# Kernel tuning notes

Measured on AMD Instinct MI355X. Metric: run time of the kernel, lower is better.

Reference implementation:

```python
import jax, jax.numpy as jnp
import numpy as np

B, S, N, E = 2048, 5, 80, 592
FX, FF, FE, D = 8, 4, 8, 8
H = 800  # GRU hidden


def setup_inputs() -> dict:
    key = jax.random.key(0)
    ks = jax.random.split(key, 20)
    inp = {
        "x": jax.random.normal(ks[0], (B, S, N, FX), jnp.float32),
        "edge_index": jax.random.randint(ks[1], (B, S, 2, E), 0, N, jnp.int32),
        "edge_f": jax.random.normal(ks[2], (B, S, E, FF), jnp.float32),
        "edge_attr": jax.random.normal(ks[3], (B, S, E, FE), jnp.float32),
        # GNN (net_ResEG) params
        "Wx": jax.random.normal(ks[4], (FX, D), jnp.float32) * 0.1,
        "We": jax.random.normal(ks[5], (FE, D), jnp.float32) * 0.1,
        "Wf": jax.random.normal(ks[6], (FF, D), jnp.float32) * 0.1,
        "Wedge": jax.random.normal(ks[7], (2 * D + FE, D), jnp.float32) * 0.1,
        # GRU params (PyTorch layout: [3H, in])
        "w_ih": jax.random.normal(ks[8], (3 * H, N * D + E * D), jnp.float32) * 0.02,
        "w_hh": jax.random.normal(ks[9], (3 * H, H), jnp.float32) * 0.02,
        "b_ih": jnp.zeros((3 * H,), jnp.float32),
        "b_hh": jnp.zeros((3 * H,), jnp.float32),
        # MLP params
        "mlp_w1": jax.random.normal(ks[10], (S * H, 1280), jnp.float32) * 0.02,
        "mlp_b1": jnp.zeros((1280,), jnp.float32),
        "mlp_w2": jax.random.normal(ks[11], (1280, S * 80), jnp.float32) * 0.02,
        "mlp_b2": jnp.zeros((S * 80,), jnp.float32),
    }
    return inp


def _gnn(xg, eig, efg, eag, Wx, We, Wf, Wedge):
    # one graph: xg [N,FX], eig [2,E], efg [E,FF], eag [E,FE]
    src, dst = eig[0], eig[1]
    m = jax.nn.relu(eag @ We + efg @ Wf)            # [E,D] edge messages
    agg = jnp.zeros((N, D), m.dtype).at[dst].add(m)  # scatter-add to nodes
    x_out = xg + jax.nn.relu(xg @ Wx + agg)          # residual node update [N,D]
    feat = jnp.concatenate([x_out[src], x_out[dst], eag], axis=-1)  # [E,2D+FE]
    e_out = eag + jax.nn.relu(feat @ Wedge)          # residual edge update [E,D]
    return x_out, e_out


def _forward(x, edge_index, edge_f, edge_attr, Wx, We, Wf, Wedge,
             w_ih, w_hh, b_ih, b_hh, mlp_w1, mlp_b1, mlp_w2, mlp_b2):
    # normalize edge indices (edge_index[i,j] - edge_index[i,j,0].min())
    mins = edge_index[:, :, 0, :].min(axis=-1)[:, :, None, None]  # [B,S,1,1]
    ei = edge_index - mins

    flat = lambda a: a.reshape((B * S,) + a.shape[2:])
    x1, e1 = jax.vmap(lambda a, b, c, d: _gnn(a, b, c, d, Wx, We, Wf, Wedge))(
        flat(x), flat(ei), flat(edge_f), flat(edge_attr))
    x1 = x1.reshape(B, S, N * D)
    e1 = e1.reshape(B, S, E * D)
    seq = jnp.concatenate([x1, e1], axis=2)  # [B,S,5376]

    # single-layer GRU, batch_first (dropout inactive for 1 layer)
    def step(h, xt):
        gi = xt @ w_ih.T + b_ih   # [B,3H]
        gh = h @ w_hh.T + b_hh
        ir, iz, inn = jnp.split(gi, 3, axis=-1)
        hr, hz, hn = jnp.split(gh, 3, axis=-1)
        r = jax.nn.sigmoid(ir + hr)
        z = jax.nn.sigmoid(iz + hz)
        n = jnp.tanh(inn + r * hn)
        h_new = (1.0 - z) * n + z * h
        return h_new, h_new

    h0 = jnp.zeros((B, H), seq.dtype)
    _, ys = jax.lax.scan(step, h0, jnp.swapaxes(seq, 0, 1))  # [S,B,H]
    y = jnp.swapaxes(ys, 0, 1).reshape(B, S * H)             # [B,4000]

    y = y @ mlp_w1 + mlp_b1
    y = y @ mlp_w2 + mlp_b2
    return y.reshape(B, 80, 5)


def reference(x, edge_index, edge_f, edge_attr, Wx, We, Wf, Wedge,
              w_ih, w_hh, b_ih, b_hh, mlp_w1, mlp_b1, mlp_w2, mlp_b2):
    return _forward(x, edge_index, edge_f, edge_attr, Wx, We, Wf, Wedge,
                    w_ih, w_hh, b_ih, b_hh, mlp_w1, mlp_b1, mlp_w2, mlp_b2)
```

## Files before the change

kernel.cpp:

```cpp
#include <hip/hip_runtime.h>
#include <math.h>

constexpr int B_  = 2048;
constexpr int S_  = 5;
constexpr int N_  = 80;
constexpr int E_  = 592;
constexpr int FX_ = 8;
constexpr int FF_ = 4;
constexpr int FE_ = 8;
constexpr int D_  = 8;
constexpr int H_  = 800;

constexpr int BS_  = B_ * S_;
constexpr int XD_  = N_ * D_;
constexpr int ED_  = E_ * D_;
constexpr int SEQ_ = XD_ + ED_;
constexpr int G3_  = 3 * H_;
constexpr int MIN_ = S_ * H_;
constexpr int MH_  = 1280;
constexpr int MO_  = S_ * 80;

typedef __bf16 bf16_t;
typedef __bf16 bf16x8 __attribute__((ext_vector_type(8)));
typedef float  f32x4  __attribute__((ext_vector_type(4)));

__device__ __forceinline__ float sigmoidf_(float x) {
    return 1.0f / (1.0f + expf(-x));
}

__device__ __forceinline__ void async16(const void* g, void* l) {
    __builtin_amdgcn_global_load_lds(
        (const __attribute__((address_space(1))) unsigned int*)g,
        (__attribute__((address_space(3))) unsigned int*)l,
        16, 0, 0);
}

__global__ __launch_bounds__(256, 4) void gnn_kernel(
    const float* __restrict__ x,
    const int*   __restrict__ ei,
    const float* __restrict__ ef,
    const float* __restrict__ ea,
    const float* __restrict__ Wx,
    const float* __restrict__ We,
    const float* __restrict__ Wf,
    const float* __restrict__ Wedge,
    bf16_t* __restrict__ seq)
{
    const int tid  = threadIdx.x;
    const int w    = tid >> 6;
    const int lane = tid & 63;
    const int g    = blockIdx.x * 4 + w;

    __shared__ float sWx[FX_ * D_];
    __shared__ float sWe[FE_ * D_];
    __shared__ float sWf[FF_ * D_];
    __shared__ float sWedge[24 * D_];
    __shared__ float agg[4][D_ * N_];
    __shared__ float su [4][D_ * N_];
    __shared__ float sv [4][D_ * N_];

    if (tid < 64) { sWx[tid] = Wx[tid]; sWe[tid] = We[tid]; }
    if (tid < 32) sWf[tid] = Wf[tid];
    if (tid < 192) sWedge[tid] = Wedge[tid];

    float* aggw = agg[w];
    float* uw   = su[w];
    float* vw   = sv[w];
    for (int i = lane; i < D_ * N_; i += 64) aggw[i] = 0.0f;

    const int* srcp = ei + (size_t)g * 2 * E_;
    const int* dstp = srcp + E_;

    int lmin = 0x7fffffff;
    for (int e = lane; e < E_; e += 64) lmin = min(lmin, srcp[e]);
    #pragma unroll
    for (int off = 32; off; off >>= 1)
        lmin = min(lmin, __shfl_xor(lmin, off, 64));
    const int mn = lmin;

    __syncthreads();

    const float* eag = ea + (size_t)g * E_ * FE_;
    const float* efg = ef + (size_t)g * E_ * FF_;
    for (int e = lane; e < E_; e += 64) {
        const float4* ap = (const float4*)(eag + (size_t)e * FE_);
        float4 a0 = ap[0], a1 = ap[1];
        float4 f0 = *(const float4*)(efg + (size_t)e * FF_);
        float a[FE_] = {a0.x, a0.y, a0.z, a0.w, a1.x, a1.y, a1.z, a1.w};
        float fv[FF_] = {f0.x, f0.y, f0.z, f0.w};

        int dadj = dstp[e] - mn;
        if (dadj < 0) dadj += N_;

        #pragma unroll
        for (int d = 0; d < D_; d++) {
            float m = 0.0f;
            #pragma unroll
            for (int k = 0; k < FE_; k++) m += a[k] * sWe[k * D_ + d];
            #pragma unroll
            for (int k = 0; k < FF_; k++) m += fv[k] * sWf[k * D_ + d];
            atomicAdd(&aggw[d * N_ + dadj], fmaxf(m, 0.0f));
        }
    }
    __syncthreads();

    const float* xg = x + (size_t)g * N_ * FX_;
    bf16_t* seqrow = seq + (size_t)g * SEQ_;
    for (int n = lane; n < N_; n += 64) {
        const float4* xp = (const float4*)(xg + (size_t)n * FX_);
        float4 x0 = xp[0], x1 = xp[1];
        float xi[FX_] = {x0.x, x0.y, x0.z, x0.w, x1.x, x1.y, x1.z, x1.w};

        float xo[D_];
        bf16x8 pk;
        #pragma unroll
        for (int d = 0; d < D_; d++) {
            float v = aggw[d * N_ + n];
            #pragma unroll
            for (int k = 0; k < FX_; k++) v += xi[k] * sWx[k * D_ + d];
            xo[d] = xi[d] + fmaxf(v, 0.0f);
            pk[d] = (bf16_t)xo[d];
        }
        *(bf16x8*)(seqrow + (size_t)n * D_) = pk;

        #pragma unroll
        for (int d = 0; d < D_; d++) {
            float uu = 0.0f, vv = 0.0f;
            #pragma unroll
            for (int k = 0; k < D_; k++) {
                uu += xo[k] * sWedge[k * D_ + d];
                vv += xo[k] * sWedge[(D_ + k) * D_ + d];
            }
            uw[d * N_ + n] = uu;
            vw[d * N_ + n] = vv;
        }
    }
    __syncthreads();

    for (int e = lane; e < E_; e += 64) {
        const float4* ap = (const float4*)(eag + (size_t)e * FE_);
        float4 a0 = ap[0], a1 = ap[1];
        float a[FE_] = {a0.x, a0.y, a0.z, a0.w, a1.x, a1.y, a1.z, a1.w};

        int sadj = srcp[e] - mn;
        int dadj = dstp[e] - mn;
        if (dadj < 0) dadj += N_;

        bf16x8 pk;
        #pragma unroll
        for (int d = 0; d < D_; d++) {
            float t = uw[d * N_ + sadj] + vw[d * N_ + dadj];
            #pragma unroll
            for (int k = 0; k < FE_; k++) t += a[k] * sWedge[(2 * D_ + k) * D_ + d];
            pk[d] = (bf16_t)(a[d] + fmaxf(t, 0.0f));
        }
        *(bf16x8*)(seqrow + XD_ + (size_t)e * D_) = pk;
    }
}

template <int TBK, typename OutT>
__global__ __launch_bounds__(256) void gemm2ph(
    const bf16_t* __restrict__ A,
    const bf16_t* __restrict__ Bm,
    const float*  __restrict__ bias,
    OutT* __restrict__ C,
    int M, int Nn, int K)
{
    constexpr int GR  = TBK / 8;
    constexpr int GM  = GR - 1;
    constexpr int RPI = 256 / GR;
    constexpr int NISS = 128 / RPI;
    constexpr int KK  = TBK / 32;

    __shared__ bf16_t As[2][128 * TBK];
    __shared__ bf16_t Bs[2][128 * TBK];

    const int tid  = threadIdx.x;
    const int wave = tid >> 6;
    const int lane = tid & 63;

    const int nbx = gridDim.x;
    int swz = blockIdx.x;
    if ((nbx & 7) == 0) {
        int cpx = nbx >> 3;
        swz = (swz & 7) * cpx + (swz >> 3);
    }
    const int ntn = (Nn + 127) >> 7;
    const int m0 = (swz / ntn) * 128;
    const int n0 = (swz % ntn) * 128;

    const int wm = (wave & 1) * 64;
    const int wn = (wave >> 1) * 64;

    const int r_loc  = tid / GR;
    const int s_slot = tid % GR;

    const int fr = lane & 15;
    const int fq = lane >> 4;

    f32x4 acc[4][4] = {};
    const int nkt = K / TBK;

    auto STAGE = [&](int t, int buf) {
        const size_t k0 = (size_t)t * TBK;
        #pragma unroll
        for (int i = 0; i < NISS; i++) {
            int row = i * RPI + r_loc;
            int gsl = s_slot ^ (row & GM);
            async16(A + (size_t)(m0 + row) * K + k0 + gsl * 8,
                    &As[buf][row * TBK + s_slot * 8]);
        }
        #pragma unroll
        for (int i = 0; i < NISS; i++) {
            int row = i * RPI + r_loc;
            int gsl = s_slot ^ (row & GM);
            int br = n0 + row; if (br > Nn - 1) br = Nn - 1;
            async16(Bm + (size_t)br * K + k0 + gsl * 8,
                    &Bs[buf][row * TBK + s_slot * 8]);
        }
    };

    STAGE(0, 0);
    asm volatile("s_waitcnt vmcnt(0)" ::: "memory");
    __builtin_amdgcn_sched_barrier(0);
    __builtin_amdgcn_s_barrier();

    for (int t = 0; t < nkt; ++t) {
        const int c = t & 1;
        int tn = t + 1; if (tn > nkt - 1) tn = nkt - 1;
        STAGE(tn, c ^ 1);

        const bf16_t* Ab = As[c];
        const bf16_t* Bb = Bs[c];
        bf16x8 af[KK][4], bfr[KK][4];
        #pragma unroll
        for (int kk = 0; kk < KK; kk++) {
            #pragma unroll
            for (int m = 0; m < 4; m++) {
                int r = wm + m * 16 + fr;
                int g = (kk * 4 + fq) ^ (r & GM);
                af[kk][m] = *(const bf16x8*)&Ab[r * TBK + g * 8];
            }
            #pragma unroll
            for (int n = 0; n < 4; n++) {
                int cc = wn + n * 16 + fr;
                int g = (kk * 4 + fq) ^ (cc & GM);
                bfr[kk][n] = *(const bf16x8*)&Bb[cc * TBK + g * 8];
            }
        }

        __builtin_amdgcn_s_setprio(1);
        #pragma unroll
        for (int kk = 0; kk < KK; kk++)
            #pragma unroll
            for (int m = 0; m < 4; m++)
                #pragma unroll
                for (int n = 0; n < 4; n++)
                    acc[m][n] = __builtin_amdgcn_mfma_f32_16x16x32_bf16(
                        af[kk][m], bfr[kk][n], acc[m][n], 0, 0, 0);
        __builtin_amdgcn_s_setprio(0);

        __builtin_amdgcn_sched_barrier(0);
        asm volatile("s_waitcnt vmcnt(0)" ::: "memory");
        __builtin_amdgcn_sched_barrier(0);
        __builtin_amdgcn_s_barrier();
    }

    const int crow = fq * 4;
    #pragma unroll
    for (int m = 0; m < 4; m++) {
        #pragma unroll
        for (int n = 0; n < 4; n++) {
            int row = m0 + wm + m * 16 + crow;
            int col = n0 + wn + n * 16 + fr;
            if (col < Nn) {
                float bv = bias[col];
                #pragma unroll
                for (int r = 0; r < 4; r++) {
                    float v = acc[m][n][r] + bv;
                    C[(size_t)(row + r) * Nn + col] = (OutT)v;
                }
            }
        }
    }
}

__global__ __launch_bounds__(256) void f2bf_kernel(
    const float* __restrict__ in, bf16_t* __restrict__ out, int n)
{
    int i = (blockIdx.x * 256 + threadIdx.x) * 4;
    if (i + 3 < n) {
        float4 v = *(const float4*)&in[i];
        out[i + 0] = (bf16_t)v.x;
        out[i + 1] = (bf16_t)v.y;
        out[i + 2] = (bf16_t)v.z;
        out[i + 3] = (bf16_t)v.w;
    } else {
        for (; i < n; i++) out[i] = (bf16_t)in[i];
    }
}

__global__ __launch_bounds__(256) void tconv_kernel(
    const float* __restrict__ in, bf16_t* __restrict__ out, int K, int N)
{
    __shared__ float tile[32][33];
    int k0 = blockIdx.y * 32, n0 = blockIdx.x * 32;
    int tx = threadIdx.x & 31, ty = threadIdx.x >> 5;
    #pragma unroll
    for (int r = 0; r < 32; r += 8) {
        int k = k0 + ty + r, n = n0 + tx;
        tile[ty + r][tx] = (k < K && n < N) ? in[(size_t)k * N + n] : 0.0f;
    }
    __syncthreads();
    #pragma unroll
    for (int r = 0; r < 32; r += 8) {
        int n = n0 + ty + r, k = k0 + tx;
        if (n < N && k < K) out[(size_t)n * K + k] = (bf16_t)tile[tx][ty + r];
    }
}

__global__ __launch_bounds__(256) void gru_gates_kernel(
    const float* __restrict__ gi,
    const float* __restrict__ gh,
    float*  __restrict__ h,
    bf16_t* __restrict__ hb,
    bf16_t* __restrict__ yb,
    int t)
{
    int i = blockIdx.x * blockDim.x + threadIdx.x;
    if (i >= B_ * H_) return;
    int b = i / H_;
    int j = i - b * H_;
    const float* girow = gi + ((size_t)b * S_ + t) * G3_;
    const float* ghrow = gh + (size_t)b * G3_;
    float r = sigmoidf_(girow[j] + ghrow[j]);
    float z = sigmoidf_(girow[H_ + j] + ghrow[H_ + j]);
    float n = tanhf(girow[2 * H_ + j] + r * ghrow[2 * H_ + j]);
    float hp = h[i];
    float hn = (1.0f - z) * n + z * hp;
    h[i] = hn;
    hb[i] = (bf16_t)hn;
    yb[(size_t)b * MIN_ + t * H_ + j] = (bf16_t)hn;
}

extern "C" void kernel_launch(void* const* d_in, const int* in_sizes, int n_in,
                              void* d_out, int out_size, void* d_ws, size_t ws_size,
                              hipStream_t stream) {
    const float* x     = (const float*)d_in[0];
    const int*   ei    = (const int*)  d_in[1];
    const float* ef    = (const float*)d_in[2];
    const float* ea    = (const float*)d_in[3];
    const float* Wx    = (const float*)d_in[4];
    const float* We    = (const float*)d_in[5];
    const float* Wf    = (const float*)d_in[6];
    const float* Wedge = (const float*)d_in[7];
    const float* w_ih  = (const float*)d_in[8];
    const float* w_hh  = (const float*)d_in[9];
    const float* b_ih  = (const float*)d_in[10];
    const float* b_hh  = (const float*)d_in[11];
    const float* w1    = (const float*)d_in[12];
    const float* b1    = (const float*)d_in[13];
    const float* w2    = (const float*)d_in[14];
    const float* b2    = (const float*)d_in[15];
    float* out = (float*)d_out;

    char* p = (char*)d_ws;
    auto alloc = [&](size_t bytes) {
        void* r = (void*)p;
        p += (bytes + 255) & ~(size_t)255;
        return r;
    };
    bf16_t* seq   = (bf16_t*)alloc((size_t)BS_ * SEQ_ * 2);
    bf16_t* wihb  = (bf16_t*)alloc((size_t)G3_ * SEQ_ * 2);
    bf16_t* whhb  = (bf16_t*)alloc((size_t)G3_ * H_ * 2);
    bf16_t* w1t   = (bf16_t*)alloc((size_t)MH_ * MIN_ * 2);
    bf16_t* w2t   = (bf16_t*)alloc((size_t)MO_ * MH_ * 2);
    float*  gi    = (float*) alloc((size_t)BS_ * G3_ * 4);
    float*  gh    = (float*) alloc((size_t)B_ * G3_ * 4);
    float*  h     = (float*) alloc((size_t)B_ * H_ * 4);
    bf16_t* hb    = (bf16_t*)alloc((size_t)B_ * H_ * 2);
    bf16_t* yb    = (bf16_t*)alloc((size_t)B_ * MIN_ * 2);
    bf16_t* t1b   = (bf16_t*)alloc((size_t)B_ * MH_ * 2);

    hipMemsetAsync(h,  0, (size_t)B_ * H_ * sizeof(float), stream);
    hipMemsetAsync(hb, 0, (size_t)B_ * H_ * sizeof(bf16_t), stream);

    {
        int n = G3_ * SEQ_;
        f2bf_kernel<<<(n / 4 + 255) / 256, 256, 0, stream>>>(w_ih, wihb, n);
    }
    {
        int n = G3_ * H_;
        f2bf_kernel<<<(n / 4 + 255) / 256, 256, 0, stream>>>(w_hh, whhb, n);
    }
    {
        dim3 grid((MH_ + 31) / 32, (MIN_ + 31) / 32);
        tconv_kernel<<<grid, 256, 0, stream>>>(w1, w1t, MIN_, MH_);
    }
    {
        dim3 grid((MO_ + 31) / 32, (MH_ + 31) / 32);
        tconv_kernel<<<grid, 256, 0, stream>>>(w2, w2t, MH_, MO_);
    }

    gnn_kernel<<<BS_ / 4, 256, 0, stream>>>(x, ei, ef, ea, Wx, We, Wf, Wedge, seq);

    {
        int nblocks = (BS_ / 128) * ((G3_ + 127) / 128);
        gemm2ph<64, float><<<nblocks, 256, 0, stream>>>(seq, wihb, b_ih, gi, BS_, G3_, SEQ_);
    }

    for (int t = 0; t < S_; t++) {
        int nblocks = (B_ / 128) * ((G3_ + 127) / 128);
        gemm2ph<32, float><<<nblocks, 256, 0, stream>>>(hb, whhb, b_hh, gh, B_, G3_, H_);
        gru_gates_kernel<<<(B_ * H_ + 255) / 256, 256, 0, stream>>>(gi, gh, h, hb, yb, t);
    }

    {
        int nblocks = (B_ / 128) * ((MH_ + 127) / 128);
        gemm2ph<32, bf16_t><<<nblocks, 256, 0, stream>>>(yb, w1t, b1, t1b, B_, MH_, MIN_);
    }
    {
        int nblocks = (B_ / 128) * ((MO_ + 127) / 128);
        gemm2ph<32, float><<<nblocks, 256, 0, stream>>>(t1b, w2t, b2, out, B_, MO_, MH_);
    }
}
```

Measured before the change: 1.413 ms.

## Restructure GNN kernel with wave-local sync, edge prefetch and vectorized LDS

Rewrites the per-graph GNN kernel so each wave loads its own copy of the weights into shared memory. Block-wide __syncthreads barriers are replaced with wave-local lgkmcnt waits, which works because each wave owns its own graph. The edge loops are software-pipelined so the next edge's global loads are issued before the current edge's math. Weight reads become float4 LDS loads, and the u/v node projections are stored node-major with padding so each edge gathers them in four vector loads. This targets memory latency and barrier stalls in the GNN stage but relies on wave-level ordering of LDS operations and drops the occupancy hint in launch bounds.

```diff
diff --git a/kernel.cpp b/kernel.cpp
--- a/kernel.cpp
+++ b/kernel.cpp
@@ -35,7 +35,12 @@
         16, 0, 0);
 }
 
-__global__ __launch_bounds__(256, 4) void gnn_kernel(
+__device__ __forceinline__ void fma4(float4& a, float s, const float* w) {
+    float4 ww = *(const float4*)w;
+    a.x += s * ww.x; a.y += s * ww.y; a.z += s * ww.z; a.w += s * ww.w;
+}
+
+__global__ __launch_bounds__(256) void gnn_kernel(
     const float* __restrict__ x,
     const int*   __restrict__ ei,
     const float* __restrict__ ef,
@@ -46,27 +51,27 @@
     const float* __restrict__ Wedge,
     bf16_t* __restrict__ seq)
 {
+    constexpr int UVP = 20;
     const int tid  = threadIdx.x;
     const int w    = tid >> 6;
     const int lane = tid & 63;
     const int g    = blockIdx.x * 4 + w;
 
-    __shared__ float sWx[FX_ * D_];
-    __shared__ float sWe[FE_ * D_];
-    __shared__ float sWf[FF_ * D_];
-    __shared__ float sWedge[24 * D_];
+    __shared__ float sW[352];
     __shared__ float agg[4][D_ * N_];
-    __shared__ float su [4][D_ * N_];
-    __shared__ float sv [4][D_ * N_];
-
-    if (tid < 64) { sWx[tid] = Wx[tid]; sWe[tid] = We[tid]; }
-    if (tid < 32) sWf[tid] = Wf[tid];
-    if (tid < 192) sWedge[tid] = Wedge[tid];
+    __shared__ float uv [4][N_ * UVP];
+
+    sW[160 + lane]       = Wedge[lane];
+    sW[160 + 64 + lane]  = Wedge[64 + lane];
+    sW[160 + 128 + lane] = Wedge[128 + lane];
+    sW[lane]      = Wx[lane];
+    sW[64 + lane] = We[lane];
+    if (lane < 32) sW[128 + lane] = Wf[lane];
 
     float* aggw = agg[w];
-    float* uw   = su[w];
-    float* vw   = sv[w];
-    for (int i = lane; i < D_ * N_; i += 64) aggw[i] = 0.0f;
+    float* uvw  = uv[w];
+    #pragma unroll
+    for (int i = 0; i < 10; i++) aggw[lane + i * 64] = 0.0f;
 
     const int* srcp = ei + (size_t)g * 2 * E_;
     const int* dstp = srcp + E_;
@@ -78,84 +83,156 @@
         lmin = min(lmin, __shfl_xor(lmin, off, 64));
     const int mn = lmin;
 
-    __syncthreads();
+    asm volatile("s_waitcnt lgkmcnt(0)" ::: "memory");
 
     const float* eag = ea + (size_t)g * E_ * FE_;
     const float* efg = ef + (size_t)g * E_ * FF_;
-    for (int e = lane; e < E_; e += 64) {
-        const float4* ap = (const float4*)(eag + (size_t)e * FE_);
-        float4 a0 = ap[0], a1 = ap[1];
-        float4 f0 = *(const float4*)(efg + (size_t)e * FF_);
-        float a[FE_] = {a0.x, a0.y, a0.z, a0.w, a1.x, a1.y, a1.z, a1.w};
-        float fv[FF_] = {f0.x, f0.y, f0.z, f0.w};
-
-        int dadj = dstp[e] - mn;
-        if (dadj < 0) dadj += N_;
-
-        #pragma unroll
-        for (int d = 0; d < D_; d++) {
-            float m = 0.0f;
-            #pragma unroll
-            for (int k = 0; k < FE_; k++) m += a[k] * sWe[k * D_ + d];
-            #pragma unroll
-            for (int k = 0; k < FF_; k++) m += fv[k] * sWf[k * D_ + d];
-            atomicAdd(&aggw[d * N_ + dadj], fmaxf(m, 0.0f));
-        }
-    }
-    __syncthreads();
+    const float* sWe_ = sW + 64;
+    const float* sWf_ = sW + 128;
+
+    auto edge_msg = [&](float4 a0, float4 a1, float4 f, int dn) {
+        float aa[8]  = {a0.x, a0.y, a0.z, a0.w, a1.x, a1.y, a1.z, a1.w};
+        float ffv[4] = {f.x, f.y, f.z, f.w};
+        float4 mlo = {0, 0, 0, 0}, mhi = {0, 0, 0, 0};
+        #pragma unroll
+        for (int k = 0; k < 8; k++) {
+            fma4(mlo, aa[k], &sWe_[k * 8]);
+            fma4(mhi, aa[k], &sWe_[k * 8 + 4]);
+        }
+        #pragma unroll
+        for (int k = 0; k < 4; k++) {
+            fma4(mlo, ffv[k], &sWf_[k * 8]);
+            fma4(mhi, ffv[k], &sWf_[k * 8 + 4]);
+        }
+        atomicAdd(&aggw[0 * N_ + dn], fmaxf(mlo.x, 0.0f));
+        atomicAdd(&aggw[1 * N_ + dn], fmaxf(mlo.y, 0.0f));
+        atomicAdd(&aggw[2 * N_ + dn], fmaxf(mlo.z, 0.0f));
+        atomicAdd(&aggw[3 * N_ + dn], fmaxf(mlo.w, 0.0f));
+        atomicAdd(&aggw[4 * N_ + dn], fmaxf(mhi.x, 0.0f));
+        atomicAdd(&aggw[5 * N_ + dn], fmaxf(mhi.y, 0.0f));
+        atomicAdd(&aggw[6 * N_ + dn], fmaxf(mhi.z, 0.0f));
+        atomicAdd(&aggw[7 * N_ + dn], fmaxf(mhi.w, 0.0f));
+    };
+
+    float4 ca0, ca1, cf; int cdn;
+    {
+        const float4* ap = (const float4*)(eag + (size_t)lane * FE_);
+        ca0 = ap[0]; ca1 = ap[1];
+        cf  = *(const float4*)(efg + (size_t)lane * FF_);
+        int dd = dstp[lane] - mn; if (dd < 0) dd += N_;
+        cdn = dd;
+    }
+    for (int i = 0; i < 9; i++) {
+        int en = lane + (i + 1) * 64;
+        int ec = (en < E_) ? en : 0;
+        const float4* ap = (const float4*)(eag + (size_t)ec * FE_);
+        float4 na0 = ap[0], na1 = ap[1];
+        float4 nf  = *(const float4*)(efg + (size_t)ec * FF_);
+        int dd = dstp[ec] - mn; if (dd < 0) dd += N_;
+
+        edge_msg(ca0, ca1, cf, cdn);
+        ca0 = na0; ca1 = na1; cf = nf; cdn = dd;
+    }
+    if (lane < 16) edge_msg(ca0, ca1, cf, cdn);
+
+    asm volatile("s_waitcnt lgkmcnt(0)" ::: "memory");
 
     const float* xg = x + (size_t)g * N_ * FX_;
     bf16_t* seqrow = seq + (size_t)g * SEQ_;
-    for (int n = lane; n < N_; n += 64) {
-        const float4* xp = (const float4*)(xg + (size_t)n * FX_);
-        float4 x0 = xp[0], x1 = xp[1];
-        float xi[FX_] = {x0.x, x0.y, x0.z, x0.w, x1.x, x1.y, x1.z, x1.w};
-
-        float xo[D_];
+    const float* sWx_  = sW;
+    const float* sWu_  = sW + 160;
+    const float* sWv_  = sW + 160 + 64;
+    #pragma unroll
+    for (int it = 0; it < 2; it++) {
+        int n = lane + it * 64;
+        if (n < N_) {
+            const float4* xp = (const float4*)(xg + (size_t)n * FX_);
+            float4 x0 = xp[0], x1 = xp[1];
+            float xi[8] = {x0.x, x0.y, x0.z, x0.w, x1.x, x1.y, x1.z, x1.w};
+
+            float4 vlo = {aggw[0 * N_ + n], aggw[1 * N_ + n],
+                          aggw[2 * N_ + n], aggw[3 * N_ + n]};
+            float4 vhi = {aggw[4 * N_ + n], aggw[5 * N_ + n],
+                          aggw[6 * N_ + n], aggw[7 * N_ + n]};
+            #pragma unroll
+            for (int k = 0; k < 8; k++) {
+                fma4(vlo, xi[k], &sWx_[k * 8]);
+                fma4(vhi, xi[k], &sWx_[k * 8 + 4]);
+            }
+            float xo[8];
+            xo[0] = xi[0] + fmaxf(vlo.x, 0.0f); xo[1] = xi[1] + fmaxf(vlo.y, 0.0f);
+            xo[2] = xi[2] + fmaxf(vlo.z, 0.0f); xo[3] = xi[3] + fmaxf(vlo.w, 0.0f);
+            xo[4] = xi[4] + fmaxf(vhi.x, 0.0f); xo[5] = xi[5] + fmaxf(vhi.y, 0.0f);
+            xo[6] = xi[6] + fmaxf(vhi.z, 0.0f); xo[7] = xi[7] + fmaxf(vhi.w, 0.0f);
+
+            bf16x8 pk;
+            #pragma unroll
+            for (int d = 0; d < 8; d++) pk[d] = (bf16_t)xo[d];
+            *(bf16x8*)(seqrow + (size_t)n * D_) = pk;
+
+            float4 ulo = {0,0,0,0}, uhi = {0,0,0,0};
+            float4 wlo = {0,0,0,0}, whi = {0,0,0,0};
+            #pragma unroll
+            for (int k = 0; k < 8; k++) {
+                fma4(ulo, xo[k], &sWu_[k * 8]);
+                fma4(uhi, xo[k], &sWu_[k * 8 + 4]);
+                fma4(wlo, xo[k], &sWv_[k * 8]);
+                fma4(whi, xo[k], &sWv_[k * 8 + 4]);
+            }
+            *(float4*)&uvw[n * UVP + 0]  = ulo;
+            *(float4*)&uvw[n * UVP + 4]  = uhi;
+            *(float4*)&uvw[n * UVP + 8]  = wlo;
+            *(float4*)&uvw[n * UVP + 12] = whi;
+        }
+    }
+    asm volatile("s_waitcnt lgkmcnt(0)" ::: "memory");
+
+    const float* sW3 = sW + 160 + 128;
+    auto edge_upd = [&](float4 a0, float4 a1, int sn, int dn, int e) {
+        float aa[8] = {a0.x, a0.y, a0.z, a0.w, a1.x, a1.y, a1.z, a1.w};
+        float4 tlo = *(const float4*)&uvw[sn * UVP];
+        float4 thi = *(const float4*)&uvw[sn * UVP + 4];
+        float4 qlo = *(const float4*)&uvw[dn * UVP + 8];
+        float4 qhi = *(const float4*)&uvw[dn * UVP + 12];
+        tlo.x += qlo.x; tlo.y += qlo.y; tlo.z += qlo.z; tlo.w += qlo.w;
+        thi.x += qhi.x; thi.y += qhi.y; thi.z += qhi.z; thi.w += qhi.w;
+        #pragma unroll
+        for (int k = 0; k < 8; k++) {
+            fma4(tlo, aa[k], &sW3[k * 8]);
+            fma4(thi, aa[k], &sW3[k * 8 + 4]);
+        }
         bf16x8 pk;
-        #pragma unroll
-        for (int d = 0; d < D_; d++) {
-            float v = aggw[d * N_ + n];
-            #pragma unroll
-            for (int k = 0; k < FX_; k++) v += xi[k] * sWx[k * D_ + d];
-            xo[d] = xi[d] + fmaxf(v, 0.0f);
-            pk[d] = (bf16_t)xo[d];
-        }
-        *(bf16x8*)(seqrow + (size_t)n * D_) = pk;
-
-        #pragma unroll
-        for (int d = 0; d < D_; d++) {
-            float uu = 0.0f, vv = 0.0f;
-            #pragma unroll
-            for (int k = 0; k < D_; k++) {
-                uu += xo[k] * sWedge[k * D_ + d];
-                vv += xo[k] * sWedge[(D_ + k) * D_ + d];
-            }
-            uw[d * N_ + n] = uu;
-            vw[d * N_ + n] = vv;
-        }
-    }
-    __syncthreads();
-
-    for (int e = lane; e < E_; e += 64) {
-        const float4* ap = (const float4*)(eag + (size_t)e * FE_);
-        float4 a0 = ap[0], a1 = ap[1];
-        float a[FE_] = {a0.x, a0.y, a0.z, a0.w, a1.x, a1.y, a1.z, a1.w};
-
-        int sadj = srcp[e] - mn;
-        int dadj = dstp[e] - mn;
-        if (dadj < 0) dadj += N_;
-
-        bf16x8 pk;
-        #pragma unroll
-        for (int d = 0; d < D_; d++) {
-            float t = uw[d * N_ + sadj] + vw[d * N_ + dadj];
-            #pragma unroll
-            for (int k = 0; k < FE_; k++) t += a[k] * sWedge[(2 * D_ + k) * D_ + d];
-            pk[d] = (bf16_t)(a[d] + fmaxf(t, 0.0f));
-        }
+        pk[0] = (bf16_t)(aa[0] + fmaxf(tlo.x, 0.0f));
+        pk[1] = (bf16_t)(aa[1] + fmaxf(tlo.y, 0.0f));
+        pk[2] = (bf16_t)(aa[2] + fmaxf(tlo.z, 0.0f));
+        pk[3] = (bf16_t)(aa[3] + fmaxf(tlo.w, 0.0f));
+        pk[4] = (bf16_t)(aa[4] + fmaxf(thi.x, 0.0f));
+        pk[5] = (bf16_t)(aa[5] + fmaxf(thi.y, 0.0f));
+        pk[6] = (bf16_t)(aa[6] + fmaxf(thi.z, 0.0f));
+        pk[7] = (bf16_t)(aa[7] + fmaxf(thi.w, 0.0f));
         *(bf16x8*)(seqrow + XD_ + (size_t)e * D_) = pk;
-    }
+    };
+
+    int csn, cdn2;
+    {
+        const float4* ap = (const float4*)(eag + (size_t)lane * FE_);
+        ca0 = ap[0]; ca1 = ap[1];
+        csn = srcp[lane] - mn;
+        int dd = dstp[lane] - mn; if (dd < 0) dd += N_;
+        cdn2 = dd;
+    }
+    for (int i = 0; i < 9; i++) {
+        int en = lane + (i + 1) * 64;
+        int ec = (en < E_) ? en : 0;
+        const float4* ap = (const float4*)(eag + (size_t)ec * FE_);
+        float4 na0 = ap[0], na1 = ap[1];
+        int nsn = srcp[ec] - mn;
+        int dd = dstp[ec] - mn; if (dd < 0) dd += N_;
+
+        edge_upd(ca0, ca1, csn, cdn2, lane + i * 64);
+        ca0 = na0; ca1 = na1; csn = nsn; cdn2 = dd;
+    }
+    if (lane < 16) edge_upd(ca0, ca1, csn, cdn2, 576 + lane);
 }
 
 template <int TBK, typename OutT>
```

Result: faster. 1.341 ms (-5.1%).
